# Optimization experiments

Hardware: AMD Instinct MI355X
Metric: run time of the kernel (lower is better)

## Reference

```python
import math
import jax, jax.numpy as jnp
import numpy as np

VOCAB = 50257
MAX_SEQ = 64
D_MODEL = 1024
N_HEADS = 16
N_LAYERS = 12
BATCH = 256
SEQ = 64


def setup_inputs() -> dict:
    key = jax.random.key(0)
    ks = jax.random.split(key, 16)
    s = 0.02
    d, L = D_MODEL, N_LAYERS
    inp = {
        "idx": jax.random.randint(ks[0], (BATCH, SEQ), 0, VOCAB, dtype=jnp.int32),
        "tok_emb": jax.random.normal(ks[1], (VOCAB, d), jnp.float32) * s,
        "pos_emb": jax.random.normal(ks[2], (MAX_SEQ, d), jnp.float32) * s,
        # per-block params stacked over layer dim [L, ...]; linear as x @ W + b
        "wqkv": jax.random.normal(ks[3], (L, d, 3 * d), jnp.float32) * s,
        "bqkv": jnp.zeros((L, 3 * d), jnp.float32),
        "wo": jax.random.normal(ks[4], (L, d, d), jnp.float32) * s,
        "bo": jnp.zeros((L, d), jnp.float32),
        "w1": jax.random.normal(ks[5], (L, d, 4 * d), jnp.float32) * s,
        "b1": jnp.zeros((L, 4 * d), jnp.float32),
        "w2": jax.random.normal(ks[6], (L, 4 * d, d), jnp.float32) * s,
        "b2": jnp.zeros((L, d), jnp.float32),
        "ln_g": jnp.ones((d,), jnp.float32),
        "ln_b": jnp.zeros((d,), jnp.float32),
        "out_w": jax.random.normal(ks[7], (d, d), jnp.float32) * s,
        "out_b": jnp.zeros((d,), jnp.float32),
    }
    return inp


def _attention(x, wqkv_l, bqkv_l, wo_l, bo_l):
    B, S, d = x.shape
    H = N_HEADS
    dh = d // H
    qkv = x @ wqkv_l + bqkv_l                      # [B,S,3d]
    q, k, v = jnp.split(qkv, 3, axis=-1)
    q = q.reshape(B, S, H, dh).transpose(0, 2, 1, 3)  # [B,H,S,dh]
    k = k.reshape(B, S, H, dh).transpose(0, 2, 1, 3)
    v = v.reshape(B, S, H, dh).transpose(0, 2, 1, 3)
    # NOTE: original scales by sqrt(d_model), not sqrt(head_dim)
    attn = jnp.einsum("bhqd,bhkd->bhqk", q, k) / math.sqrt(d)
    causal = jnp.tril(jnp.ones((S, S), bool))       # query i attends key j<=i
    attn = jnp.where(causal[None, None], attn, -jnp.inf)
    # NOTE: original applies softmax over dim=-2 (the QUERY axis)
    attn = jax.nn.softmax(attn, axis=-2)
    y = jnp.einsum("bhqk,bhkd->bhqd", attn, v)      # [B,H,S,dh]
    y = y.transpose(0, 2, 1, 3).reshape(B, S, d)
    return y @ wo_l + bo_l


def _layer_norm(x, g, b, eps=1e-5):
    mu = jnp.mean(x, axis=-1, keepdims=True)
    var = jnp.var(x, axis=-1, keepdims=True)
    return (x - mu) * jax.lax.rsqrt(var + eps) * g + b


def reference(idx, tok_emb, pos_emb, wqkv, bqkv, wo, bo, w1, b1, w2, b2,
              ln_g, ln_b, out_w, out_b):
    S = idx.shape[1]
    x = tok_emb[idx] + pos_emb[:S]                 # [B,S,d]
    for l in range(N_LAYERS):
        x = _attention(x, wqkv[l], bqkv[l], wo[l], bo[l]) + x
        h = jax.nn.gelu(x @ w1[l] + b1[l], approximate=False)
        x = h @ w2[l] + b2[l] + x
    x = _layer_norm(x, ln_g, ln_b)
    return x @ out_w + out_b
```

## Files before the change

kernel.cpp:

```cpp
#include <hip/hip_runtime.h>
#include <stdint.h>

typedef unsigned short u16;
typedef __bf16 bf16x8 __attribute__((ext_vector_type(8)));
typedef float f32x4 __attribute__((ext_vector_type(4)));

#define MT 16384

__device__ __forceinline__ u16 f2bf(float f) {
  union { float f; unsigned u; } x; x.f = f;
  unsigned r = x.u + 0x7fffu + ((x.u >> 16) & 1u);
  return (u16)(r >> 16);
}

#pragma clang diagnostic push
#pragma clang diagnostic ignored "-Waddress-space-conversion"
typedef __attribute__((address_space(1))) unsigned as1u;
typedef __attribute__((address_space(3))) unsigned as3u;
__device__ __forceinline__ void stage16(const u16* g, u16* lbase) {
  __builtin_amdgcn_global_load_lds((as1u*)g, (as3u*)lbase, 16, 0, 0);
}
#pragma clang diagnostic pop

__global__ void __launch_bounds__(256)
transpose_cvt(const float* __restrict__ in, u16* __restrict__ out, int K, int N) {
  __shared__ float tile[32][33];
  const int k0 = blockIdx.y * 32, n0 = blockIdx.x * 32;
  const int tx = threadIdx.x, ty = threadIdx.y;
  #pragma unroll
  for (int r = 0; r < 32; r += 8)
    tile[ty + r][tx] = in[(size_t)(k0 + ty + r) * N + n0 + tx];
  __syncthreads();
  #pragma unroll
  for (int r = 0; r < 32; r += 8)
    out[(size_t)(n0 + ty + r) * K + k0 + tx] = f2bf(tile[tx][ty + r]);
}

__global__ void __launch_bounds__(256)
embed_kernel(const int* __restrict__ idx, const float* __restrict__ tok,
             const float* __restrict__ pos, float* __restrict__ x,
             u16* __restrict__ xb) {
  const int tk = blockIdx.x;
  const int s = tk & 63;
  const int id = idx[tk];
  const int t = threadIdx.x;
  float4 a = ((const float4*)(tok + (size_t)id * 1024))[t];
  float4 p = ((const float4*)(pos + (size_t)s * 1024))[t];
  float4 r; r.x = a.x + p.x; r.y = a.y + p.y; r.z = a.z + p.z; r.w = a.w + p.w;
  ((float4*)(x + (size_t)tk * 1024))[t] = r;
  u16* o = xb + (size_t)tk * 1024 + t * 4;
  o[0] = f2bf(r.x); o[1] = f2bf(r.y); o[2] = f2bf(r.z); o[3] = f2bf(r.w);
}

template<int EPI>
__global__ void __launch_bounds__(512, 2)
gemm256(const u16* __restrict__ A, const u16* __restrict__ Bt,
        const float* __restrict__ bias, float* __restrict__ resf,
        u16* __restrict__ outb, float* __restrict__ outf,
        int M, int N, int K, int gn) {
  __shared__ __align__(16) u16 lds[2][2][16384];
  const int t = threadIdx.x;
  const int lane = t & 63, w = t >> 6;
  const int wr = w >> 2, wc = w & 3;
  const int fr = lane & 15, fg = lane >> 4;

  const int nwg = gridDim.x;
  const int bid = blockIdx.x;
  const int s = (bid & 7) * (nwg >> 3) + (bid >> 3);
  const int tn = s % gn, tm = s / gn;
  const int m0 = tm * 256, n0 = tn * 256;

  const int srow = w * 8 + (lane >> 3);
  const int sg = (lane & 7) ^ (lane >> 3);
  const u16* gA[4]; const u16* gB[4];
  #pragma unroll
  for (int c = 0; c < 4; ++c) {
    gA[c] = A  + (size_t)(m0 + c * 64 + srow) * K + sg * 8;
    gB[c] = Bt + (size_t)(n0 + c * 64 + srow) * K + sg * 8;
  }
  const int lofs = w * 512;

  f32x4 acc[8][4] = {};
  const int NT = K >> 6;

  #pragma unroll
  for (int c = 0; c < 4; ++c) {
    stage16(gA[c], &lds[0][0][lofs + c * 4096]);
    stage16(gB[c], &lds[0][1][lofs + c * 4096]);
  }
  __syncthreads();

  int cur = 0;
  for (int kt = 0; kt < NT; ++kt) {
    if (kt + 1 < NT) {
      const int koff = (kt + 1) << 6;
      #pragma unroll
      for (int c = 0; c < 4; ++c) {
        stage16(gA[c] + koff, &lds[cur ^ 1][0][lofs + c * 4096]);
        stage16(gB[c] + koff, &lds[cur ^ 1][1][lofs + c * 4096]);
      }
    }
    #pragma unroll
    for (int h = 0; h < 2; ++h) {
      bf16x8 af[8], bv[4];
      #pragma unroll
      for (int m = 0; m < 8; ++m) {
        const int row = wr * 128 + m * 16 + fr;
        const int g = (fg + h * 4) ^ (fr & 7);
        af[m] = *(const bf16x8*)&lds[cur][0][row * 64 + g * 8];
      }
      #pragma unroll
      for (int n = 0; n < 4; ++n) {
        const int row = wc * 64 + n * 16 + fr;
        const int g = (fg + h * 4) ^ (fr & 7);
        bv[n] = *(const bf16x8*)&lds[cur][1][row * 64 + g * 8];
      }
      #pragma unroll
      for (int m = 0; m < 8; ++m)
        #pragma unroll
        for (int n = 0; n < 4; ++n)
          acc[m][n] = __builtin_amdgcn_mfma_f32_16x16x32_bf16(af[m], bv[n], acc[m][n], 0, 0, 0);
    }
    __syncthreads();
    cur ^= 1;
  }

  #pragma unroll
  for (int m = 0; m < 8; ++m) {
    const int row = m0 + wr * 128 + m * 16 + fg * 4;
    #pragma unroll
    for (int n = 0; n < 4; ++n) {
      const int col = n0 + wc * 64 + n * 16 + fr;
      const float bc = bias[col];
      #pragma unroll
      for (int i = 0; i < 4; ++i) {
        const size_t off = (size_t)(row + i) * N + col;
        float v = acc[m][n][i] + bc;
        if constexpr (EPI == 0) {
          outb[off] = f2bf(v);
        } else if constexpr (EPI == 1) {
          v = 0.5f * v * (1.0f + erff(v * 0.70710678118654752f));
          outb[off] = f2bf(v);
        } else if constexpr (EPI == 2) {
          v += resf[off];
          resf[off] = v;
          outb[off] = f2bf(v);
        } else {
          outf[off] = v;
        }
      }
    }
  }
}

__global__ void __launch_bounds__(256)
attn_kernel(const u16* __restrict__ qkv, u16* __restrict__ y) {
  __shared__ __align__(16) u16 qs[64][72];
  __shared__ __align__(16) u16 ks[64][72];
  __shared__ __align__(16) u16 vts[64][72];
  __shared__ __align__(16) float S[64][68];
  __shared__ float red[4][64];

  const int h = blockIdx.x, b = blockIdx.y;
  const int t = threadIdx.x;
  const int lane = t & 63, w = t >> 6;
  const int fr = lane & 15, fg = lane >> 4;

  #pragma unroll
  for (int it = 0; it < 2; ++it) {
    const int id = t + it * 256;
    const int row = id >> 3, seg = id & 7;
    const size_t gq = (size_t)(b * 64 + row) * 3072 + h * 64 + seg * 8;
    *(uint4*)&qs[row][seg * 8] = *(const uint4*)&qkv[gq];
    *(uint4*)&ks[row][seg * 8] = *(const uint4*)&qkv[gq + 1024];
  }
  {
    const int d = t & 63;
    #pragma unroll
    for (int it = 0; it < 16; ++it) {
      const int s = (t >> 6) + it * 4;
      vts[d][s] = qkv[(size_t)(b * 64 + s) * 3072 + 2048 + h * 64 + d];
    }
  }
  __syncthreads();

  f32x4 sa[4] = {};
  #pragma unroll
  for (int kk = 0; kk < 64; kk += 32) {
    bf16x8 qa = *(const bf16x8*)&qs[w * 16 + fr][kk + fg * 8];
    #pragma unroll
    for (int n = 0; n < 4; ++n) {
      bf16x8 kb = *(const bf16x8*)&ks[n * 16 + fr][kk + fg * 8];
      sa[n] = __builtin_amdgcn_mfma_f32_16x16x32_bf16(qa, kb, sa[n], 0, 0, 0);
    }
  }
  #pragma unroll
  for (int n = 0; n < 4; ++n)
    #pragma unroll
    for (int i = 0; i < 4; ++i) {
      const int row = w * 16 + fg * 4 + i, col = n * 16 + fr;
      S[row][col] = (row >= col) ? sa[n][i] * 0.03125f : -1e30f;
    }
  __syncthreads();

  const int c = t & 63, q4 = t >> 6;
  float mx = -1e30f;
  float e[16];
  #pragma unroll
  for (int i = 0; i < 16; ++i) mx = fmaxf(mx, S[q4 * 16 + i][c]);
  red[q4][c] = mx;
  __syncthreads();
  mx = fmaxf(fmaxf(red[0][c], red[1][c]), fmaxf(red[2][c], red[3][c]));
  float sum = 0.f;
  #pragma unroll
  for (int i = 0; i < 16; ++i) { e[i] = __expf(S[q4 * 16 + i][c] - mx); sum += e[i]; }
  __syncthreads();
  red[q4][c] = sum;
  __syncthreads();
  sum = red[0][c] + red[1][c] + red[2][c] + red[3][c];
  const float inv = 1.0f / sum;
  u16 (*P)[72] = qs;
  #pragma unroll
  for (int i = 0; i < 16; ++i)
    P[q4 * 16 + i][c] = f2bf(e[i] * inv);
  __syncthreads();

  f32x4 oa[4] = {};
  #pragma unroll
  for (int kk = 0; kk < 64; kk += 32) {
    bf16x8 pa = *(const bf16x8*)&P[w * 16 + fr][kk + fg * 8];
    #pragma unroll
    for (int n = 0; n < 4; ++n) {
      bf16x8 vb = *(const bf16x8*)&vts[n * 16 + fr][kk + fg * 8];
      oa[n] = __builtin_amdgcn_mfma_f32_16x16x32_bf16(pa, vb, oa[n], 0, 0, 0);
    }
  }
  #pragma unroll
  for (int n = 0; n < 4; ++n)
    #pragma unroll
    for (int i = 0; i < 4; ++i) {
      const int row = w * 16 + fg * 4 + i, col = n * 16 + fr;
      y[(size_t)(b * 64 + row) * 1024 + h * 64 + col] = f2bf(oa[n][i]);
    }
}

__global__ void __launch_bounds__(256)
ln_kernel(const float* __restrict__ x, const float* __restrict__ g,
          const float* __restrict__ bb, u16* __restrict__ xn) {
  __shared__ float sred[8];
  const int tok = blockIdx.x;
  const int t = threadIdx.x;
  const float4 v = ((const float4*)(x + (size_t)tok * 1024))[t];
  float s  = v.x + v.y + v.z + v.w;
  float ss = v.x * v.x + v.y * v.y + v.z * v.z + v.w * v.w;
  #pragma unroll
  for (int o = 32; o > 0; o >>= 1) {
    s  += __shfl_xor(s, o);
    ss += __shfl_xor(ss, o);
  }
  const int w = t >> 6;
  if ((t & 63) == 0) { sred[w] = s; sred[4 + w] = ss; }
  __syncthreads();
  s  = sred[0] + sred[1] + sred[2] + sred[3];
  ss = sred[4] + sred[5] + sred[6] + sred[7];
  const float mu = s * (1.0f / 1024.0f);
  const float var = ss * (1.0f / 1024.0f) - mu * mu;
  const float rs = rsqrtf(var + 1e-5f);
  const float4 gg = ((const float4*)g)[t];
  const float4 b4 = ((const float4*)bb)[t];
  u16* o = xn + (size_t)tok * 1024 + t * 4;
  o[0] = f2bf((v.x - mu) * rs * gg.x + b4.x);
  o[1] = f2bf((v.y - mu) * rs * gg.y + b4.y);
  o[2] = f2bf((v.z - mu) * rs * gg.z + b4.z);
  o[3] = f2bf((v.w - mu) * rs * gg.w + b4.w);
}

extern "C" void kernel_launch(void* const* d_in, const int* in_sizes, int n_in,
                              void* d_out, int out_size, void* d_ws, size_t ws_size,
                              hipStream_t stream) {
  const int*   idx     = (const int*)  d_in[0];
  const float* tok_emb = (const float*)d_in[1];
  const float* pos_emb = (const float*)d_in[2];
  const float* wqkv    = (const float*)d_in[3];
  const float* bqkv    = (const float*)d_in[4];
  const float* wo      = (const float*)d_in[5];
  const float* bo      = (const float*)d_in[6];
  const float* w1      = (const float*)d_in[7];
  const float* b1      = (const float*)d_in[8];
  const float* w2      = (const float*)d_in[9];
  const float* b2      = (const float*)d_in[10];
  const float* ln_g    = (const float*)d_in[11];
  const float* ln_b    = (const float*)d_in[12];
  const float* out_w   = (const float*)d_in[13];
  const float* out_b   = (const float*)d_in[14];

  char* p = (char*)d_ws;
  auto take = [&](size_t n) { char* r = p; p += (n + 255) & ~(size_t)255; return r; };
  u16*   wqkv_t = (u16*)  take((size_t)1024 * 3072 * 2);
  u16*   wo_t   = (u16*)  take((size_t)1024 * 1024 * 2);
  u16*   w1_t   = (u16*)  take((size_t)1024 * 4096 * 2);
  u16*   w2_t   = (u16*)  take((size_t)4096 * 1024 * 2);
  u16*   wout_t = (u16*)  take((size_t)1024 * 1024 * 2);
  float* xf     = (float*)take((size_t)MT * 1024 * 4);
  u16*   xb     = (u16*)  take((size_t)MT * 1024 * 2);
  u16*   yb     = (u16*)  take((size_t)MT * 1024 * 2);
  u16*   big    = (u16*)  take((size_t)MT * 4096 * 2);

  const dim3 tb(32, 8);
  embed_kernel<<<MT, 256, 0, stream>>>(idx, tok_emb, pos_emb, xf, xb);

  for (int l = 0; l < 12; ++l) {
    transpose_cvt<<<dim3(3072 / 32, 1024 / 32), tb, 0, stream>>>(
        wqkv + (size_t)l * 1024 * 3072, wqkv_t, 1024, 3072);
    transpose_cvt<<<dim3(1024 / 32, 1024 / 32), tb, 0, stream>>>(
        wo + (size_t)l * 1024 * 1024, wo_t, 1024, 1024);
    transpose_cvt<<<dim3(4096 / 32, 1024 / 32), tb, 0, stream>>>(
        w1 + (size_t)l * 1024 * 4096, w1_t, 1024, 4096);
    transpose_cvt<<<dim3(1024 / 32, 4096 / 32), tb, 0, stream>>>(
        w2 + (size_t)l * 4096 * 1024, w2_t, 4096, 1024);

    gemm256<0><<<(MT / 256) * (3072 / 256), 512, 0, stream>>>(
        xb, wqkv_t, bqkv + (size_t)l * 3072,
        nullptr, big, nullptr, MT, 3072, 1024, 3072 / 256);
    attn_kernel<<<dim3(16, 256), 256, 0, stream>>>(big, yb);
    gemm256<2><<<(MT / 256) * (1024 / 256), 512, 0, stream>>>(
        yb, wo_t, bo + (size_t)l * 1024,
        xf, xb, nullptr, MT, 1024, 1024, 1024 / 256);
    gemm256<1><<<(MT / 256) * (4096 / 256), 512, 0, stream>>>(
        xb, w1_t, b1 + (size_t)l * 4096,
        nullptr, big, nullptr, MT, 4096, 1024, 4096 / 256);
    gemm256<2><<<(MT / 256) * (1024 / 256), 512, 0, stream>>>(
        big, w2_t, b2 + (size_t)l * 1024,
        xf, xb, nullptr, MT, 1024, 4096, 1024 / 256);
  }

  transpose_cvt<<<dim3(1024 / 32, 1024 / 32), tb, 0, stream>>>(out_w, wout_t, 1024, 1024);
  ln_kernel<<<MT, 256, 0, stream>>>(xf, ln_g, ln_b, yb);
  gemm256<3><<<(MT / 256) * (1024 / 256), 512, 0, stream>>>(
      yb, wout_t, out_b, nullptr, nullptr, (float*)d_out, MT, 1024, 1024, 1024 / 256);
}
```

Before: 6.906 ms.

## Replace 256x256 GEMM tile with 128x256 tile, 4 waves, BK=32

Measured after the change: 7.462 ms. +8.0%, slower.

```diff
diff --git a/kernel.cpp b/kernel.cpp
--- a/kernel.cpp
+++ b/kernel.cpp
@@ -53,84 +53,75 @@
 }
 
 template<int EPI>
-__global__ void __launch_bounds__(512, 2)
-gemm256(const u16* __restrict__ A, const u16* __restrict__ Bt,
-        const float* __restrict__ bias, float* __restrict__ resf,
-        u16* __restrict__ outb, float* __restrict__ outf,
-        int M, int N, int K, int gn) {
-  __shared__ __align__(16) u16 lds[2][2][16384];
+__global__ void __launch_bounds__(256, 3)
+gemm128x256(const u16* __restrict__ A, const u16* __restrict__ Bt,
+            const float* __restrict__ bias, float* __restrict__ resf,
+            u16* __restrict__ outb, float* __restrict__ outf,
+            int M, int N, int K, int gn) {
+  __shared__ __align__(16) u16 lA[2][4096];
+  __shared__ __align__(16) u16 lB[2][8192];
   const int t = threadIdx.x;
   const int lane = t & 63, w = t >> 6;
-  const int wr = w >> 2, wc = w & 3;
   const int fr = lane & 15, fg = lane >> 4;
 
   const int nwg = gridDim.x;
   const int bid = blockIdx.x;
   const int s = (bid & 7) * (nwg >> 3) + (bid >> 3);
   const int tn = s % gn, tm = s / gn;
-  const int m0 = tm * 256, n0 = tn * 256;
-
-  const int srow = w * 8 + (lane >> 3);
-  const int sg = (lane & 7) ^ (lane >> 3);
-  const u16* gA[4]; const u16* gB[4];
-  #pragma unroll
-  for (int c = 0; c < 4; ++c) {
-    gA[c] = A  + (size_t)(m0 + c * 64 + srow) * K + sg * 8;
-    gB[c] = Bt + (size_t)(n0 + c * 64 + srow) * K + sg * 8;
-  }
-  const int lofs = w * 512;
+  const int m0 = tm * 128, n0 = tn * 256;
+
+  const int rin = ((lane >> 3) << 1) + ((lane >> 2) & 1);
+  const int fgl = (lane & 3) ^ ((lane >> 3) & 3);
+  const u16* gA[2]; const u16* gB[4];
+  #pragma unroll
+  for (int i = 0; i < 2; ++i)
+    gA[i] = A + (size_t)(m0 + (w * 2 + i) * 16 + rin) * K + fgl * 8;
+  #pragma unroll
+  for (int j = 0; j < 4; ++j)
+    gB[j] = Bt + (size_t)(n0 + (w * 4 + j) * 16 + rin) * K + fgl * 8;
+
+  const int sub8 = ((fr & 1) * 4 + (fg ^ ((fr >> 1) & 3))) * 8;
+  const int ar = (fr >> 1) * 64 + sub8;
+  const int br = (w * 32 + (fr >> 1)) * 64 + sub8;
 
   f32x4 acc[8][4] = {};
-  const int NT = K >> 6;
-
-  #pragma unroll
-  for (int c = 0; c < 4; ++c) {
-    stage16(gA[c], &lds[0][0][lofs + c * 4096]);
-    stage16(gB[c], &lds[0][1][lofs + c * 4096]);
-  }
+  const int NT = K >> 5;
+
+  #pragma unroll
+  for (int i = 0; i < 2; ++i) stage16(gA[i], &lA[0][(w * 2 + i) * 512]);
+  #pragma unroll
+  for (int j = 0; j < 4; ++j) stage16(gB[j], &lB[0][(w * 4 + j) * 512]);
   __syncthreads();
 
   int cur = 0;
   for (int kt = 0; kt < NT; ++kt) {
     if (kt + 1 < NT) {
-      const int koff = (kt + 1) << 6;
+      const int ko = (kt + 1) << 5;
       #pragma unroll
-      for (int c = 0; c < 4; ++c) {
-        stage16(gA[c] + koff, &lds[cur ^ 1][0][lofs + c * 4096]);
-        stage16(gB[c] + koff, &lds[cur ^ 1][1][lofs + c * 4096]);
-      }
-    }
-    #pragma unroll
-    for (int h = 0; h < 2; ++h) {
-      bf16x8 af[8], bv[4];
+      for (int i = 0; i < 2; ++i) stage16(gA[i] + ko, &lA[cur ^ 1][(w * 2 + i) * 512]);
       #pragma unroll
-      for (int m = 0; m < 8; ++m) {
-        const int row = wr * 128 + m * 16 + fr;
-        const int g = (fg + h * 4) ^ (fr & 7);
-        af[m] = *(const bf16x8*)&lds[cur][0][row * 64 + g * 8];
-      }
+      for (int j = 0; j < 4; ++j) stage16(gB[j] + ko, &lB[cur ^ 1][(w * 4 + j) * 512]);
+    }
+    bf16x8 af[8], bv[4];
+    #pragma unroll
+    for (int m = 0; m < 8; ++m) af[m] = *(const bf16x8*)&lA[cur][m * 512 + ar];
+    #pragma unroll
+    for (int n = 0; n < 4; ++n) bv[n] = *(const bf16x8*)&lB[cur][n * 512 + br];
+    #pragma unroll
+    for (int m = 0; m < 8; ++m)
       #pragma unroll
-      for (int n = 0; n < 4; ++n) {
-        const int row = wc * 64 + n * 16 + fr;
-        const int g = (fg + h * 4) ^ (fr & 7);
-        bv[n] = *(const bf16x8*)&lds[cur][1][row * 64 + g * 8];
-      }
-      #pragma unroll
-      for (int m = 0; m < 8; ++m)
-        #pragma unroll
-        for (int n = 0; n < 4; ++n)
-          acc[m][n] = __builtin_amdgcn_mfma_f32_16x16x32_bf16(af[m], bv[n], acc[m][n], 0, 0, 0);
-    }
+      for (int n = 0; n < 4; ++n)
+        acc[m][n] = __builtin_amdgcn_mfma_f32_16x16x32_bf16(af[m], bv[n], acc[m][n], 0, 0, 0);
     __syncthreads();
     cur ^= 1;
   }
 
   #pragma unroll
   for (int m = 0; m < 8; ++m) {
-    const int row = m0 + wr * 128 + m * 16 + fg * 4;
+    const int row = m0 + m * 16 + fg * 4;
     #pragma unroll
     for (int n = 0; n < 4; ++n) {
-      const int col = n0 + wc * 64 + n * 16 + fr;
+      const int col = n0 + w * 64 + n * 16 + fr;
       const float bc = bias[col];
       #pragma unroll
       for (int i = 0; i < 4; ++i) {
@@ -319,23 +310,23 @@
     transpose_cvt<<<dim3(1024 / 32, 4096 / 32), tb, 0, stream>>>(
         w2 + (size_t)l * 4096 * 1024, w2_t, 4096, 1024);
 
-    gemm256<0><<<(MT / 256) * (3072 / 256), 512, 0, stream>>>(
+    gemm128x256<0><<<(MT / 128) * (3072 / 256), 256, 0, stream>>>(
         xb, wqkv_t, bqkv + (size_t)l * 3072,
         nullptr, big, nullptr, MT, 3072, 1024, 3072 / 256);
     attn_kernel<<<dim3(16, 256), 256, 0, stream>>>(big, yb);
-    gemm256<2><<<(MT / 256) * (1024 / 256), 512, 0, stream>>>(
+    gemm128x256<2><<<(MT / 128) * (1024 / 256), 256, 0, stream>>>(
         yb, wo_t, bo + (size_t)l * 1024,
         xf, xb, nullptr, MT, 1024, 1024, 1024 / 256);
-    gemm256<1><<<(MT / 256) * (4096 / 256), 512, 0, stream>>>(
+    gemm128x256<1><<<(MT / 128) * (4096 / 256), 256, 0, stream>>>(
         xb, w1_t, b1 + (size_t)l * 4096,
         nullptr, big, nullptr, MT, 4096, 1024, 4096 / 256);
-    gemm256<2><<<(MT / 256) * (1024 / 256), 512, 0, stream>>>(
+    gemm128x256<2><<<(MT / 128) * (1024 / 256), 256, 0, stream>>>(
         big, w2_t, b2 + (size_t)l * 1024,
         xf, xb, nullptr, MT, 1024, 4096, 1024 / 256);
   }
 
   transpose_cvt<<<dim3(1024 / 32, 1024 / 32), tb, 0, stream>>>(out_w, wout_t, 1024, 1024);
   ln_kernel<<<MT, 256, 0, stream>>>(xf, ln_g, ln_b, yb);
-  gemm256<3><<<(MT / 256) * (1024 / 256), 512, 0, stream>>>(
+  gemm128x256<3><<<(MT / 128) * (1024 / 256), 256, 0, stream>>>(
       yb, wout_t, out_b, nullptr, nullptr, (float*)d_out, MT, 1024, 1024, 1024 / 256);
 }
```

## Rewrite GEMM main loop as a four-phase ping-pong pipeline with fine-grained waits

Applied to the files above, without the earlier changes.

New measurement: 7.261 ms. +5.1%, slower.

```diff
diff --git a/kernel.cpp b/kernel.cpp
--- a/kernel.cpp
+++ b/kernel.cpp
@@ -17,7 +17,7 @@
 #pragma clang diagnostic ignored "-Waddress-space-conversion"
 typedef __attribute__((address_space(1))) unsigned as1u;
 typedef __attribute__((address_space(3))) unsigned as3u;
-__device__ __forceinline__ void stage16(const u16* g, u16* lbase) {
+__device__ __forceinline__ void stage16(const u16* g, const u16* lbase) {
   __builtin_amdgcn_global_load_lds((as1u*)g, (as3u*)lbase, 16, 0, 0);
 }
 #pragma clang diagnostic pop
@@ -53,12 +53,12 @@
 }
 
 template<int EPI>
-__global__ void __launch_bounds__(512, 2)
-gemm256(const u16* __restrict__ A, const u16* __restrict__ Bt,
-        const float* __restrict__ bias, float* __restrict__ resf,
-        u16* __restrict__ outb, float* __restrict__ outf,
-        int M, int N, int K, int gn) {
-  __shared__ __align__(16) u16 lds[2][2][16384];
+__global__ void __launch_bounds__(512, 1)
+gemm256p(const u16* __restrict__ A, const u16* __restrict__ Bt,
+         const float* __restrict__ bias, float* __restrict__ resf,
+         u16* __restrict__ outb, float* __restrict__ outf,
+         int M, int N, int K, int gn) {
+  __shared__ __align__(16) u16 lds[65536];
   const int t = threadIdx.x;
   const int lane = t & 63, w = t >> 6;
   const int wr = w >> 2, wc = w & 3;
@@ -66,64 +66,105 @@
 
   const int nwg = gridDim.x;
   const int bid = blockIdx.x;
-  const int s = (bid & 7) * (nwg >> 3) + (bid >> 3);
-  const int tn = s % gn, tm = s / gn;
+  const int sw = (bid & 7) * (nwg >> 3) + (bid >> 3);
+  const int tn = sw % gn, tm = sw / gn;
   const int m0 = tm * 256, n0 = tn * 256;
 
-  const int srow = w * 8 + (lane >> 3);
-  const int sg = (lane & 7) ^ (lane >> 3);
-  const u16* gA[4]; const u16* gB[4];
-  #pragma unroll
-  for (int c = 0; c < 4; ++c) {
-    gA[c] = A  + (size_t)(m0 + c * 64 + srow) * K + sg * 8;
-    gB[c] = Bt + (size_t)(n0 + c * 64 + srow) * K + sg * 8;
-  }
-  const int lofs = w * 512;
+  const int srow = w * 32 + (lane >> 2);
+  const int scol = (lane & 3) * 8;
+  const u16* gA0 = A  + (size_t)(m0 + srow) * K + scol;
+  const u16* gA1 = A  + (size_t)(m0 + srow + 16) * K + scol;
+  const u16* gB0 = Bt + (size_t)(n0 + srow) * K + scol;
+  const u16* gB1 = Bt + (size_t)(n0 + srow + 16) * K + scol;
+  const int dA = w * 1024;
+  const int dB = 16384 + w * 1024;
 
   f32x4 acc[8][4] = {};
   const int NT = K >> 6;
 
-  #pragma unroll
-  for (int c = 0; c < 4; ++c) {
-    stage16(gA[c], &lds[0][0][lofs + c * 4096]);
-    stage16(gB[c], &lds[0][1][lofs + c * 4096]);
-  }
-  __syncthreads();
+  auto STAGE_A = [&](int b, int kh, int ko) {
+    stage16(gA0 + ko + kh * 32, &lds[b * 32768 + kh * 8192 + dA]);
+    stage16(gA1 + ko + kh * 32, &lds[b * 32768 + kh * 8192 + dA + 512]);
+  };
+  auto STAGE_B = [&](int b, int kh, int ko) {
+    stage16(gB0 + ko + kh * 32, &lds[b * 32768 + kh * 8192 + dB]);
+    stage16(gB1 + ko + kh * 32, &lds[b * 32768 + kh * 8192 + dB + 512]);
+  };
+  auto LDA4 = [&](bf16x8* af, int mq, int kh, int c) {
+    #pragma unroll
+    for (int m = 0; m < 4; ++m)
+      af[m] = *(const bf16x8*)&lds[c * 32768 + kh * 8192 +
+                                   (wr * 128 + (mq * 4 + m) * 16 + fr) * 32 + fg * 8];
+  };
+  auto LDB4 = [&](bf16x8* bv, int kh, int c) {
+    #pragma unroll
+    for (int n = 0; n < 4; ++n)
+      bv[n] = *(const bf16x8*)&lds[c * 32768 + 16384 + kh * 8192 +
+                                   (wc * 64 + n * 16 + fr) * 32 + fg * 8];
+  };
+  auto MFMA16 = [&](bf16x8* af, bf16x8* bv, int mq) {
+    __builtin_amdgcn_s_setprio(1);
+    #pragma unroll
+    for (int m = 0; m < 4; ++m)
+      #pragma unroll
+      for (int n = 0; n < 4; ++n)
+        acc[mq * 4 + m][n] =
+            __builtin_amdgcn_mfma_f32_16x16x32_bf16(af[m], bv[n], acc[mq * 4 + m][n], 0, 0, 0);
+    __builtin_amdgcn_s_setprio(0);
+  };
+  #define BARRIER() __builtin_amdgcn_s_barrier()
+  #define LGKM0()  asm volatile("s_waitcnt lgkmcnt(0)" ::: "memory")
+  #define VMCNT4() asm volatile("s_waitcnt vmcnt(4)" ::: "memory")
+
+  STAGE_A(0, 0, 0); STAGE_B(0, 0, 0);
+  STAGE_A(0, 1, 0); STAGE_B(0, 1, 0);
+  VMCNT4();
+  BARRIER();
 
   int cur = 0;
-  for (int kt = 0; kt < NT; ++kt) {
-    if (kt + 1 < NT) {
-      const int koff = (kt + 1) << 6;
-      #pragma unroll
-      for (int c = 0; c < 4; ++c) {
-        stage16(gA[c] + koff, &lds[cur ^ 1][0][lofs + c * 4096]);
-        stage16(gB[c] + koff, &lds[cur ^ 1][1][lofs + c * 4096]);
-      }
-    }
-    #pragma unroll
-    for (int h = 0; h < 2; ++h) {
-      bf16x8 af[8], bv[4];
-      #pragma unroll
-      for (int m = 0; m < 8; ++m) {
-        const int row = wr * 128 + m * 16 + fr;
-        const int g = (fg + h * 4) ^ (fr & 7);
-        af[m] = *(const bf16x8*)&lds[cur][0][row * 64 + g * 8];
-      }
-      #pragma unroll
-      for (int n = 0; n < 4; ++n) {
-        const int row = wc * 64 + n * 16 + fr;
-        const int g = (fg + h * 4) ^ (fr & 7);
-        bv[n] = *(const bf16x8*)&lds[cur][1][row * 64 + g * 8];
-      }
-      #pragma unroll
-      for (int m = 0; m < 8; ++m)
-        #pragma unroll
-        for (int n = 0; n < 4; ++n)
-          acc[m][n] = __builtin_amdgcn_mfma_f32_16x16x32_bf16(af[m], bv[n], acc[m][n], 0, 0, 0);
-    }
-    __syncthreads();
-    cur ^= 1;
-  }
+  for (int u = 0; u < NT; ++u) {
+    const int ko = (u + 1 < NT) ? (u + 1) << 6 : 0;
+    const int nb = cur ^ 1;
+    bf16x8 bv[4];
+    {
+      bf16x8 af[4];
+      LDA4(af, 0, 0, cur); LDB4(bv, 0, cur);
+      STAGE_A(nb, 0, ko);
+      BARRIER(); LGKM0();
+      MFMA16(af, bv, 0);
+      BARRIER();
+    }
+    {
+      bf16x8 af[4];
+      LDA4(af, 1, 0, cur);
+      STAGE_B(nb, 0, ko);
+      VMCNT4();
+      BARRIER(); LGKM0();
+      MFMA16(af, bv, 1);
+      BARRIER();
+    }
+    {
+      bf16x8 af[4];
+      LDA4(af, 0, 1, cur); LDB4(bv, 1, cur);
+      STAGE_A(nb, 1, ko);
+      BARRIER(); LGKM0();
+      MFMA16(af, bv, 0);
+      BARRIER();
+    }
+    {
+      bf16x8 af[4];
+      LDA4(af, 1, 1, cur);
+      STAGE_B(nb, 1, ko);
+      VMCNT4();
+      BARRIER(); LGKM0();
+      MFMA16(af, bv, 1);
+      BARRIER();
+    }
+    cur = nb;
+  }
+  #undef BARRIER
+  #undef LGKM0
+  #undef VMCNT4
 
   #pragma unroll
   for (int m = 0; m < 8; ++m) {
@@ -319,23 +360,23 @@
     transpose_cvt<<<dim3(1024 / 32, 4096 / 32), tb, 0, stream>>>(
         w2 + (size_t)l * 4096 * 1024, w2_t, 4096, 1024);
 
-    gemm256<0><<<(MT / 256) * (3072 / 256), 512, 0, stream>>>(
+    gemm256p<0><<<(MT / 256) * (3072 / 256), 512, 0, stream>>>(
         xb, wqkv_t, bqkv + (size_t)l * 3072,
         nullptr, big, nullptr, MT, 3072, 1024, 3072 / 256);
     attn_kernel<<<dim3(16, 256), 256, 0, stream>>>(big, yb);
-    gemm256<2><<<(MT / 256) * (1024 / 256), 512, 0, stream>>>(
+    gemm256p<2><<<(MT / 256) * (1024 / 256), 512, 0, stream>>>(
         yb, wo_t, bo + (size_t)l * 1024,
         xf, xb, nullptr, MT, 1024, 1024, 1024 / 256);
-    gemm256<1><<<(MT / 256) * (4096 / 256), 512, 0, stream>>>(
+    gemm256p<1><<<(MT / 256) * (4096 / 256), 512, 0, stream>>>(
         xb, w1_t, b1 + (size_t)l * 4096,
         nullptr, big, nullptr, MT, 4096, 1024, 4096 / 256);
-    gemm256<2><<<(MT / 256) * (1024 / 256), 512, 0, stream>>>(
+    gemm256p<2><<<(MT / 256) * (1024 / 256), 512, 0, stream>>>(
         big, w2_t, b2 + (size_t)l * 1024,
         xf, xb, nullptr, MT, 1024, 4096, 1024 / 256);
   }
 
   transpose_cvt<<<dim3(1024 / 32, 1024 / 32), tb, 0, stream>>>(out_w, wout_t, 1024, 1024);
   ln_kernel<<<MT, 256, 0, stream>>>(xf, ln_g, ln_b, yb);
-  gemm256<3><<<(MT / 256) * (1024 / 256), 512, 0, stream>>>(
+  gemm256p<3><<<(MT / 256) * (1024 / 256), 512, 0, stream>>>(
       yb, wout_t, out_b, nullptr, nullptr, (float*)d_out, MT, 1024, 1024, 1024 / 256);
 }
```

## Keep residual stream in bf16 and use 128x128 GEMM tiles for FFN down-projection

Applied to the files above, without the earlier changes.

New measurement: 6.630 ms. 1.04x faster.

```diff
diff --git a/kernel.cpp b/kernel.cpp
--- a/kernel.cpp
+++ b/kernel.cpp
@@ -12,12 +12,16 @@
   unsigned r = x.u + 0x7fffu + ((x.u >> 16) & 1u);
   return (u16)(r >> 16);
 }
+__device__ __forceinline__ float bf2f(u16 b) {
+  union { float f; unsigned u; } x; x.u = ((unsigned)b) << 16;
+  return x.f;
+}
 
 #pragma clang diagnostic push
 #pragma clang diagnostic ignored "-Waddress-space-conversion"
 typedef __attribute__((address_space(1))) unsigned as1u;
 typedef __attribute__((address_space(3))) unsigned as3u;
-__device__ __forceinline__ void stage16(const u16* g, u16* lbase) {
+__device__ __forceinline__ void stage16(const u16* g, const u16* lbase) {
   __builtin_amdgcn_global_load_lds((as1u*)g, (as3u*)lbase, 16, 0, 0);
 }
 #pragma clang diagnostic pop
@@ -38,24 +42,22 @@
 
 __global__ void __launch_bounds__(256)
 embed_kernel(const int* __restrict__ idx, const float* __restrict__ tok,
-             const float* __restrict__ pos, float* __restrict__ x,
-             u16* __restrict__ xb) {
+             const float* __restrict__ pos, u16* __restrict__ xb) {
   const int tk = blockIdx.x;
   const int s = tk & 63;
   const int id = idx[tk];
   const int t = threadIdx.x;
   float4 a = ((const float4*)(tok + (size_t)id * 1024))[t];
   float4 p = ((const float4*)(pos + (size_t)s * 1024))[t];
-  float4 r; r.x = a.x + p.x; r.y = a.y + p.y; r.z = a.z + p.z; r.w = a.w + p.w;
-  ((float4*)(x + (size_t)tk * 1024))[t] = r;
   u16* o = xb + (size_t)tk * 1024 + t * 4;
-  o[0] = f2bf(r.x); o[1] = f2bf(r.y); o[2] = f2bf(r.z); o[3] = f2bf(r.w);
+  o[0] = f2bf(a.x + p.x); o[1] = f2bf(a.y + p.y);
+  o[2] = f2bf(a.z + p.z); o[3] = f2bf(a.w + p.w);
 }
 
 template<int EPI>
 __global__ void __launch_bounds__(512, 2)
 gemm256(const u16* __restrict__ A, const u16* __restrict__ Bt,
-        const float* __restrict__ bias, float* __restrict__ resf,
+        const float* __restrict__ bias, u16* __restrict__ resb,
         u16* __restrict__ outb, float* __restrict__ outf,
         int M, int N, int K, int gn) {
   __shared__ __align__(16) u16 lds[2][2][16384];
@@ -142,9 +144,101 @@
           v = 0.5f * v * (1.0f + erff(v * 0.70710678118654752f));
           outb[off] = f2bf(v);
         } else if constexpr (EPI == 2) {
-          v += resf[off];
-          resf[off] = v;
+          v += bf2f(resb[off]);
+          resb[off] = f2bf(v);
+        } else {
+          outf[off] = v;
+        }
+      }
+    }
+  }
+}
+
+template<int EPI>
+__global__ void __launch_bounds__(256, 3)
+gemm128(const u16* __restrict__ A, const u16* __restrict__ Bt,
+        const float* __restrict__ bias, u16* __restrict__ resb,
+        u16* __restrict__ outb, float* __restrict__ outf,
+        int M, int N, int K, int gn) {
+  __shared__ __align__(16) u16 lA[2][4096];
+  __shared__ __align__(16) u16 lB[2][4096];
+  const int t = threadIdx.x;
+  const int lane = t & 63, w = t >> 6;
+  const int wr = w >> 1, wc = w & 1;
+  const int fr = lane & 15, fg = lane >> 4;
+
+  const int nwg = gridDim.x;
+  const int bid = blockIdx.x;
+  const int s = (bid & 7) * (nwg >> 3) + (bid >> 3);
+  const int tn = s % gn, tm = s / gn;
+  const int m0 = tm * 128, n0 = tn * 128;
+
+  const int rin = ((lane >> 3) << 1) + ((lane >> 2) & 1);
+  const int fgl = (lane & 3) ^ ((lane >> 3) & 3);
+  const u16* gA[2]; const u16* gB[2];
+  #pragma unroll
+  for (int i = 0; i < 2; ++i) {
+    gA[i] = A  + (size_t)(m0 + (w * 2 + i) * 16 + rin) * K + fgl * 8;
+    gB[i] = Bt + (size_t)(n0 + (w * 2 + i) * 16 + rin) * K + fgl * 8;
+  }
+
+  const int sub8 = ((fr & 1) * 4 + (fg ^ ((fr >> 1) & 3))) * 8;
+  const int ar = wr * 2048 + (fr >> 1) * 64 + sub8;
+  const int br = wc * 2048 + (fr >> 1) * 64 + sub8;
+
+  f32x4 acc[4][4] = {};
+  const int NT = K >> 5;
+
+  #pragma unroll
+  for (int i = 0; i < 2; ++i) {
+    stage16(gA[i], &lA[0][(w * 2 + i) * 512]);
+    stage16(gB[i], &lB[0][(w * 2 + i) * 512]);
+  }
+  __syncthreads();
+
+  int cur = 0;
+  for (int kt = 0; kt < NT; ++kt) {
+    if (kt + 1 < NT) {
+      const int ko = (kt + 1) << 5;
+      #pragma unroll
+      for (int i = 0; i < 2; ++i) {
+        stage16(gA[i] + ko, &lA[cur ^ 1][(w * 2 + i) * 512]);
+        stage16(gB[i] + ko, &lB[cur ^ 1][(w * 2 + i) * 512]);
+      }
+    }
+    bf16x8 af[4], bv[4];
+    #pragma unroll
+    for (int m = 0; m < 4; ++m) af[m] = *(const bf16x8*)&lA[cur][ar + m * 512];
+    #pragma unroll
+    for (int n = 0; n < 4; ++n) bv[n] = *(const bf16x8*)&lB[cur][br + n * 512];
+    #pragma unroll
+    for (int m = 0; m < 4; ++m)
+      #pragma unroll
+      for (int n = 0; n < 4; ++n)
+        acc[m][n] = __builtin_amdgcn_mfma_f32_16x16x32_bf16(af[m], bv[n], acc[m][n], 0, 0, 0);
+    __syncthreads();
+    cur ^= 1;
+  }
+
+  #pragma unroll
+  for (int m = 0; m < 4; ++m) {
+    const int row = m0 + wr * 64 + m * 16 + fg * 4;
+    #pragma unroll
+    for (int n = 0; n < 4; ++n) {
+      const int col = n0 + wc * 64 + n * 16 + fr;
+      const float bc = bias[col];
+      #pragma unroll
+      for (int i = 0; i < 4; ++i) {
+        const size_t off = (size_t)(row + i) * N + col;
+        float v = acc[m][n][i] + bc;
+        if constexpr (EPI == 0) {
           outb[off] = f2bf(v);
+        } else if constexpr (EPI == 1) {
+          v = 0.5f * v * (1.0f + erff(v * 0.70710678118654752f));
+          outb[off] = f2bf(v);
+        } else if constexpr (EPI == 2) {
+          v += bf2f(resb[off]);
+          resb[off] = f2bf(v);
         } else {
           outf[off] = v;
         }
@@ -245,14 +339,15 @@
 }
 
 __global__ void __launch_bounds__(256)
-ln_kernel(const float* __restrict__ x, const float* __restrict__ g,
+ln_kernel(const u16* __restrict__ x, const float* __restrict__ g,
           const float* __restrict__ bb, u16* __restrict__ xn) {
   __shared__ float sred[8];
   const int tok = blockIdx.x;
   const int t = threadIdx.x;
-  const float4 v = ((const float4*)(x + (size_t)tok * 1024))[t];
-  float s  = v.x + v.y + v.z + v.w;
-  float ss = v.x * v.x + v.y * v.y + v.z * v.z + v.w * v.w;
+  const ushort4 raw = ((const ushort4*)(x + (size_t)tok * 1024))[t];
+  const float v0 = bf2f(raw.x), v1 = bf2f(raw.y), v2 = bf2f(raw.z), v3 = bf2f(raw.w);
+  float s  = v0 + v1 + v2 + v3;
+  float ss = v0 * v0 + v1 * v1 + v2 * v2 + v3 * v3;
   #pragma unroll
   for (int o = 32; o > 0; o >>= 1) {
     s  += __shfl_xor(s, o);
@@ -269,10 +364,10 @@
   const float4 gg = ((const float4*)g)[t];
   const float4 b4 = ((const float4*)bb)[t];
   u16* o = xn + (size_t)tok * 1024 + t * 4;
-  o[0] = f2bf((v.x - mu) * rs * gg.x + b4.x);
-  o[1] = f2bf((v.y - mu) * rs * gg.y + b4.y);
-  o[2] = f2bf((v.z - mu) * rs * gg.z + b4.z);
-  o[3] = f2bf((v.w - mu) * rs * gg.w + b4.w);
+  o[0] = f2bf((v0 - mu) * rs * gg.x + b4.x);
+  o[1] = f2bf((v1 - mu) * rs * gg.y + b4.y);
+  o[2] = f2bf((v2 - mu) * rs * gg.z + b4.z);
+  o[3] = f2bf((v3 - mu) * rs * gg.w + b4.w);
 }
 
 extern "C" void kernel_launch(void* const* d_in, const int* in_sizes, int n_in,
@@ -301,13 +396,12 @@
   u16*   w1_t   = (u16*)  take((size_t)1024 * 4096 * 2);
   u16*   w2_t   = (u16*)  take((size_t)4096 * 1024 * 2);
   u16*   wout_t = (u16*)  take((size_t)1024 * 1024 * 2);
-  float* xf     = (float*)take((size_t)MT * 1024 * 4);
   u16*   xb     = (u16*)  take((size_t)MT * 1024 * 2);
   u16*   yb     = (u16*)  take((size_t)MT * 1024 * 2);
   u16*   big    = (u16*)  take((size_t)MT * 4096 * 2);
 
   const dim3 tb(32, 8);
-  embed_kernel<<<MT, 256, 0, stream>>>(idx, tok_emb, pos_emb, xf, xb);
+  embed_kernel<<<MT, 256, 0, stream>>>(idx, tok_emb, pos_emb, xb);
 
   for (int l = 0; l < 12; ++l) {
     transpose_cvt<<<dim3(3072 / 32, 1024 / 32), tb, 0, stream>>>(
@@ -325,17 +419,17 @@
     attn_kernel<<<dim3(16, 256), 256, 0, stream>>>(big, yb);
     gemm256<2><<<(MT / 256) * (1024 / 256), 512, 0, stream>>>(
         yb, wo_t, bo + (size_t)l * 1024,
-        xf, xb, nullptr, MT, 1024, 1024, 1024 / 256);
+        xb, nullptr, nullptr, MT, 1024, 1024, 1024 / 256);
     gemm256<1><<<(MT / 256) * (4096 / 256), 512, 0, stream>>>(
         xb, w1_t, b1 + (size_t)l * 4096,
         nullptr, big, nullptr, MT, 4096, 1024, 4096 / 256);
-    gemm256<2><<<(MT / 256) * (1024 / 256), 512, 0, stream>>>(
+    gemm128<2><<<(MT / 128) * (1024 / 128), 256, 0, stream>>>(
         big, w2_t, b2 + (size_t)l * 1024,
-        xf, xb, nullptr, MT, 1024, 4096, 1024 / 256);
+        xb, nullptr, nullptr, MT, 1024, 4096, 1024 / 128);
   }
 
   transpose_cvt<<<dim3(1024 / 32, 1024 / 32), tb, 0, stream>>>(out_w, wout_t, 1024, 1024);
-  ln_kernel<<<MT, 256, 0, stream>>>(xf, ln_g, ln_b, yb);
+  ln_kernel<<<MT, 256, 0, stream>>>(xb, ln_g, ln_b, yb);
   gemm256<3><<<(MT / 256) * (1024 / 256), 512, 0, stream>>>(
       yb, wout_t, out_b, nullptr, nullptr, (float*)d_out, MT, 1024, 1024, 1024 / 256);
 }
```
